# Performance work log

Hardware: AMD Instinct MI355X
Metric: run time of the kernel (lower is better)

The kernel has to match this reference:

```python
import jax, jax.numpy as jnp
import numpy as np
import math

HID = 1024; HEADS = 8; DH = 128; CS = 200; MAXPOS = 512; K = 15; EXP = 2; MULT = 4
SCALE = DH ** -0.5
CEXP = HID * EXP  # 2048 depthwise channels


def _ln(x, g, b, eps=1e-5):
    m = jnp.mean(x, axis=-1, keepdims=True)
    v = jnp.var(x, axis=-1, keepdims=True)
    return (x - m) * jax.lax.rsqrt(v + eps) * g + b


def _ff(x, ng, nb, w1, b1, w2, b2):
    h = jax.nn.silu(_ln(x, ng, nb) @ w1 + b1)
    return h @ w2 + b2


def _attn(x, dists, ng, nb, wq, wkv, pos_emb, wo, bo):
    B, N, _ = x.shape
    x = _ln(x, ng, nb)
    nblk = math.ceil(N / CS)
    rem = N % CS
    if rem:
        x = jnp.pad(x, ((0, 0), (0, CS - rem), (0, 0)))

    def heads(t):  # [B, M*C, H*Dh] -> [B, M, H, C, Dh]
        return t.reshape(B, nblk, CS, HEADS, DH).transpose(0, 1, 3, 2, 4)

    q = heads(x @ wq)
    k, v = jnp.split(x @ wkv, 2, axis=-1)
    k, v = heads(k), heads(v)
    rel = pos_emb[dists]  # [C, C, Dh] Shaw relative position embeddings
    pos_attn = jnp.einsum('bmhcd,crd->bmhcr', q, rel) * SCALE
    if rem:
        mask = jnp.ones((CS, CS), bool).at[:rem, :rem].set(False)
        big_neg = -jnp.finfo(pos_attn.dtype).max
        pos_attn = pos_attn.at[:, -1].set(jnp.where(mask, big_neg, pos_attn[:, -1]))
    scores = jnp.einsum('bmhcd,bmhrd->bmhcr', q, k) * SCALE + pos_attn
    p = jax.nn.softmax(scores, axis=-1)
    o = jnp.einsum('bmhcr,bmhrd->bmhcd', p, v)
    o = o.transpose(0, 1, 3, 2, 4).reshape(B, nblk * CS, HEADS * DH)[:, :N]
    return o @ wo + bo


def _conv(x, ng, nb, pw1_w, pw1_b, dw_w, bn_g, bn_b, bn_m, bn_v, pw2_w, pw2_b):
    h = _ln(x, ng, nb) @ pw1_w + pw1_b            # [B, N, 2*CEXP] pointwise conv1
    a, gate = jnp.split(h, 2, axis=-1)
    h = (a * jax.nn.sigmoid(gate)).transpose(0, 2, 1)  # GLU -> [B, CEXP, N]
    pad = (K - 1) // 2
    h = jax.lax.conv_general_dilated(h, dw_w[:, None, :], (1,), [(pad, pad)],
                                     feature_group_count=CEXP,
                                     dimension_numbers=('NCH', 'OIH', 'NCH'))
    # BatchNorm1d in eval mode (running stats)
    h = (h - bn_m[:, None]) * jax.lax.rsqrt(bn_v[:, None] + 1e-5) * bn_g[:, None] + bn_b[:, None]
    h = jax.nn.silu(h).transpose(0, 2, 1)
    return h @ pw2_w + pw2_b


def setup_inputs() -> dict:
    ks = iter(jax.random.split(jax.random.key(0), 16))
    def nrm(shape, s=0.05):
        return jax.random.normal(next(ks), shape, dtype=jnp.float32) * s
    return {
        'x': jax.random.normal(next(ks), (8, 2000, HID), dtype=jnp.float32),
        'attention_dists': jax.random.randint(next(ks), (CS, CS), 0, 2 * MAXPOS + 1),
        'ff1_ng': jnp.ones((HID,)), 'ff1_nb': jnp.zeros((HID,)),
        'ff1_w1': nrm((HID, HID * MULT)), 'ff1_b1': jnp.zeros((HID * MULT,)),
        'ff1_w2': nrm((HID * MULT, HID)), 'ff1_b2': jnp.zeros((HID,)),
        'attn_ng': jnp.ones((HID,)), 'attn_nb': jnp.zeros((HID,)),
        'wq': nrm((HID, HEADS * DH)), 'wkv': nrm((HID, 2 * HEADS * DH)),
        'pos_emb': nrm((2 * MAXPOS + 1, DH)),
        'wo': nrm((HEADS * DH, HID)), 'bo': jnp.zeros((HID,)),
        'conv_ng': jnp.ones((HID,)), 'conv_nb': jnp.zeros((HID,)),
        'pw1_w': nrm((HID, 2 * CEXP)), 'pw1_b': jnp.zeros((2 * CEXP,)),
        'dw_w': nrm((CEXP, K)),
        'bn_g': jnp.ones((CEXP,)), 'bn_b': jnp.zeros((CEXP,)),
        'bn_m': jnp.zeros((CEXP,)), 'bn_v': jnp.ones((CEXP,)),
        'pw2_w': nrm((CEXP, HID)), 'pw2_b': jnp.zeros((HID,)),
        'ff2_ng': jnp.ones((HID,)), 'ff2_nb': jnp.zeros((HID,)),
        'ff2_w1': nrm((HID, HID * MULT)), 'ff2_b1': jnp.zeros((HID * MULT,)),
        'ff2_w2': nrm((HID * MULT, HID)), 'ff2_b2': jnp.zeros((HID,)),
        'post_g': jnp.ones((HID,)), 'post_b': jnp.zeros((HID,)),
    }


def reference(x, attention_dists, ff1_ng, ff1_nb, ff1_w1, ff1_b1, ff1_w2, ff1_b2,
              attn_ng, attn_nb, wq, wkv, pos_emb, wo, bo,
              conv_ng, conv_nb, pw1_w, pw1_b, dw_w, bn_g, bn_b, bn_m, bn_v, pw2_w, pw2_b,
              ff2_ng, ff2_nb, ff2_w1, ff2_b1, ff2_w2, ff2_b2, post_g, post_b):
    x = x + 0.5 * _ff(x, ff1_ng, ff1_nb, ff1_w1, ff1_b1, ff1_w2, ff1_b2)
    x = x + _attn(x, attention_dists, attn_ng, attn_nb, wq, wkv, pos_emb, wo, bo)
    x = x + _conv(x, conv_ng, conv_nb, pw1_w, pw1_b, dw_w, bn_g, bn_b, bn_m, bn_v, pw2_w, pw2_b)
    x = x + 0.5 * _ff(x, ff2_ng, ff2_nb, ff2_w1, ff2_b1, ff2_w2, ff2_b2)
    return _ln(x, post_g, post_b)
```

## Files before the change

### kernel.cpp

```cpp
#include <hip/hip_runtime.h>
#include <hip/hip_bf16.h>
#include <stdint.h>

using bf16 = __hip_bfloat16;
typedef __bf16 bf16x8v __attribute__((ext_vector_type(8)));
typedef float f32x4 __attribute__((ext_vector_type(4)));

#define MFMA16(a,b,c) __builtin_amdgcn_mfma_f32_16x16x32_bf16((a),(b),(c),0,0,0)

__device__ __forceinline__ float tof(bf16 h){ return __bfloat162float(h); }
__device__ __forceinline__ bf16 tob(float f){ return __float2bfloat16(f); }

__device__ __forceinline__ void gll16(const void* g, void* l) {
    __builtin_amdgcn_global_load_lds((const __attribute__((address_space(1))) void*)g,
                                     (__attribute__((address_space(3))) void*)l, 16, 0, 0);
}

__global__ __launch_bounds__(256)
void pad_zero(bf16* __restrict__ q, bf16* __restrict__ k, bf16* __restrict__ v)
{
    int blk = blockIdx.x, t = threadIdx.x;
    uint2 z = make_uint2(0u, 0u);
    size_t qk = (size_t)blk * 208 * 128;
    int r = 200 + (t >> 5), c = (t & 31) * 4;
    *(uint2*)(q + qk + r*128 + c) = z;
    *(uint2*)(k + qk + r*128 + c) = z;
    size_t vb = (size_t)blk * 128 * 224;
    int d = t >> 1, c0 = 200 + (t & 1) * 12;
    *(uint2*)(v + vb + d*224 + c0)     = z;
    *(uint2*)(v + vb + d*224 + c0 + 4) = z;
    *(uint2*)(v + vb + d*224 + c0 + 8) = z;
}

__global__ __launch_bounds__(256)
void cast_pe(const float* __restrict__ in, bf16* __restrict__ out, int n8)
{
    int i = blockIdx.x * 256 + threadIdx.x;
    if (i >= n8) return;
    f32x4 a = ((const f32x4*)in)[2*i], b = ((const f32x4*)in)[2*i + 1];
    union { uint4 u; bf16 h[8]; } o;
#pragma unroll
    for (int j = 0; j < 4; ++j) { o.h[j] = tob(a[j]); o.h[4+j] = tob(b[j]); }
    ((uint4*)out)[i] = o.u;
}

__global__ __launch_bounds__(256)
void transpose_cast(const float* __restrict__ in, bf16* __restrict__ out, int R, int C)
{
    __shared__ float t[32][33];
    int bx = blockIdx.x * 32, by = blockIdx.y * 32;
    int tx = threadIdx.x & 31, ty = threadIdx.x >> 5;
#pragma unroll
    for (int i = 0; i < 4; ++i)
        t[ty + i*8][tx] = in[(size_t)(by + ty + i*8) * C + bx + tx];
    __syncthreads();
#pragma unroll
    for (int i = 0; i < 4; ++i)
        out[(size_t)(bx + ty + i*8) * R + by + tx] = tob(t[tx][ty + i*8]);
}

template<bool OUT32>
__global__ __launch_bounds__(256)
void ln_k(const float* __restrict__ x, const float* __restrict__ g,
          const float* __restrict__ b, void* __restrict__ out)
{
    int row = blockIdx.x, tid = threadIdx.x;
    const float4 v = ((const float4*)(x + (size_t)row*1024))[tid];
    float s = v.x + v.y + v.z + v.w;
    float q = v.x*v.x + v.y*v.y + v.z*v.z + v.w*v.w;
#pragma unroll
    for (int m = 1; m < 64; m <<= 1) { s += __shfl_xor(s, m); q += __shfl_xor(q, m); }
    __shared__ float red[8];
    if ((tid & 63) == 0) { red[tid>>6] = s; red[4 + (tid>>6)] = q; }
    __syncthreads();
    float ts = red[0]+red[1]+red[2]+red[3];
    float tq = red[4]+red[5]+red[6]+red[7];
    float mean = ts * (1.f/1024.f);
    float var  = tq * (1.f/1024.f) - mean*mean;
    float rs = rsqrtf(var + 1e-5f);
    const float4 gv = ((const float4*)g)[tid];
    const float4 bv = ((const float4*)b)[tid];
    float o0 = (v.x-mean)*rs*gv.x + bv.x;
    float o1 = (v.y-mean)*rs*gv.y + bv.y;
    float o2 = (v.z-mean)*rs*gv.z + bv.z;
    float o3 = (v.w-mean)*rs*gv.w + bv.w;
    if (OUT32) {
        ((float4*)out)[(size_t)row*256 + tid] = make_float4(o0,o1,o2,o3);
    } else {
        bf16 tmp[4] = { tob(o0), tob(o1), tob(o2), tob(o3) };
        ((uint2*)out)[(size_t)row*256 + tid] = *(const uint2*)tmp;
    }
}

template<int EP>
__global__ __launch_bounds__(256, 2)
void gemm_bt(const bf16* __restrict__ A, const bf16* __restrict__ BT,
             int M, int N, int K, int lda,
             const float* __restrict__ bias, const float* resid, float alpha,
             void* o0, void* o1, void* o2)
{
    (void)M;
    __shared__ bf16 sA[2][4096];
    __shared__ bf16 sB[2][4096];
    const int tid = threadIdx.x;
    const int lane = tid & 63, wid = tid >> 6;
    const int wm = wid >> 1, wn = wid & 1;
    const int bn0 = blockIdx.x * 128, bm0 = blockIdx.y * 128;
    const int fr = lane & 15, fq = lane >> 4;
    const int nk = K >> 5;

    f32x4 acc[4][4];
    const f32x4 vzero = {0.f, 0.f, 0.f, 0.f};
#pragma unroll
    for (int i = 0; i < 4; ++i)
#pragma unroll
        for (int j = 0; j < 4; ++j) acc[i][j] = vzero;

    const bf16* Abase = A + (size_t)bm0 * lda;
    const bf16* Bbase = BT + (size_t)bn0 * K;

    auto stage = [&](int kb, int buf) {
#pragma unroll
        for (int rd = 0; rd < 2; ++rd) {
            int s = rd*256 + tid;
            int r = s >> 2, ko = (s & 3) * 8;
            gll16(Abase + (size_t)r*lda + kb*32 + ko, &sA[buf][s*8]);
            gll16(Bbase + (size_t)r*K   + kb*32 + ko, &sB[buf][s*8]);
        }
    };

    stage(0, 0);
    for (int kb = 0; kb < nk; ++kb) {
        __syncthreads();
        if (kb + 1 < nk) stage(kb+1, (kb+1) & 1);
        const bf16* sa = sA[kb & 1];
        const bf16* sb = sB[kb & 1];
        bf16x8v af[4], bfv[4];
#pragma unroll
        for (int mi = 0; mi < 4; ++mi)
            af[mi] = *(const bf16x8v*)(sa + (wm*64 + mi*16 + fr)*32 + fq*8);
#pragma unroll
        for (int ni = 0; ni < 4; ++ni)
            bfv[ni] = *(const bf16x8v*)(sb + (wn*64 + ni*16 + fr)*32 + fq*8);
#pragma unroll
        for (int mi = 0; mi < 4; ++mi)
#pragma unroll
            for (int ni = 0; ni < 4; ++ni)
                acc[mi][ni] = MFMA16(af[mi], bfv[ni], acc[mi][ni]);
    }

#pragma unroll
    for (int mi = 0; mi < 4; ++mi)
#pragma unroll
    for (int ni = 0; ni < 4; ++ni)
#pragma unroll
    for (int r = 0; r < 4; ++r) {
        int row = bm0 + wm*64 + mi*16 + fq*4 + r;
        int col = bn0 + wn*64 + ni*16 + fr;
        float v = acc[mi][ni][r];
        if (EP == 0) {
            v += bias[col];
            v = v * (1.f / (1.f + __expf(-v)));
            ((bf16*)o0)[(size_t)row * N + col] = tob(v);
        } else if (EP == 1) {
            v += bias[col];
            ((bf16*)o0)[(size_t)row * N + col] = tob(v);
        } else if (EP == 2) {
            float o = resid[(size_t)row * N + col] + alpha * (v + bias[col]);
            ((float*)o0)[(size_t)row * N + col] = o;
        } else {
            int sec = col >> 10, hh = (col >> 7) & 7, d = col & 127;
            int blk = (row / 200) * 8 + hh, c = row % 200;
            if (sec == 0)      ((bf16*)o0)[((size_t)blk*208 + c)*128 + d] = tob(v * 0.08838834764831845f);
            else if (sec == 1) ((bf16*)o1)[((size_t)blk*208 + c)*128 + d] = tob(v);
            else               ((bf16*)o2)[((size_t)blk*128 + d)*224 + c] = tob(v);
        }
    }
}

__global__ __launch_bounds__(64)
void pos_kernel(const bf16* __restrict__ qb, const bf16* __restrict__ peb,
                const int* __restrict__ dists, bf16* __restrict__ pbuf)
{
    const int c = blockIdx.y, mt = blockIdx.x;
    const int lane = threadIdx.x;
    const int fr = lane & 15, fq = lane >> 4;
    bf16x8v qa[4][4];
#pragma unroll
    for (int sub = 0; sub < 4; ++sub)
#pragma unroll
        for (int kk = 0; kk < 4; ++kk)
            qa[sub][kk] = *(const bf16x8v*)(qb + ((size_t)(mt*64 + sub*16 + fr)*208 + c)*128 + kk*32 + fq*8);

    for (int rt = 0; rt < 13; ++rt) {
        int r = rt*16 + fr;
        int pidx = (r < 200) ? dists[c*200 + r] : 0;
        bf16x8v bv[4];
#pragma unroll
        for (int kk = 0; kk < 4; ++kk)
            bv[kk] = *(const bf16x8v*)(peb + (size_t)pidx*128 + kk*32 + fq*8);
#pragma unroll
        for (int sub = 0; sub < 4; ++sub) {
            f32x4 a = {0.f,0.f,0.f,0.f};
#pragma unroll
            for (int kk = 0; kk < 4; ++kk) a = MFMA16(qa[sub][kk], bv[kk], a);
            int bmh = mt*64 + sub*16 + fq*4;
#pragma unroll
            for (int g = 0; g < 4; ++g)
                pbuf[((size_t)c*640 + bmh + g)*208 + r] = tob(a[g]);
        }
    }
}

__global__ __launch_bounds__(64, 4)
void attn_core(const bf16* __restrict__ qb, const bf16* __restrict__ kb,
               const bf16* __restrict__ vt, const bf16* __restrict__ pb,
               bf16* __restrict__ ob)
{
    __shared__ bf16 P[16][232];
    const int blk = blockIdx.x, qc = blockIdx.y;
    const int lane = threadIdx.x;
    const int fr = lane & 15, fq = lane >> 4;
    const size_t qkbase = (size_t)blk * 208 * 128;
    const size_t vbase  = (size_t)blk * 128 * 224;
    const int c = qc*16 + fr;

    bf16x8v qa[4];
#pragma unroll
    for (int kk = 0; kk < 4; ++kk)
        qa[kk] = *(const bf16x8v*)(qb + qkbase + (size_t)(qc*16 + fr)*128 + kk*32 + fq*8);

    f32x4 s[13];
#pragma unroll
    for (int rt = 0; rt < 13; ++rt) {
        f32x4 a = {0.f,0.f,0.f,0.f};
#pragma unroll
        for (int kk = 0; kk < 4; ++kk) {
            bf16x8v kf = *(const bf16x8v*)(kb + qkbase + (size_t)(rt*16 + fr)*128 + kk*32 + fq*8);
            a = MFMA16(kf, qa[kk], a);
        }
        s[rt] = a;
    }
#pragma unroll
    for (int rt = 0; rt < 13; ++rt) {
        if (c < 200) {
            union { uint2 u; bf16 h[4]; } pv;
            pv.u = *(const uint2*)(pb + ((size_t)c*640 + blk)*208 + rt*16 + fq*4);
#pragma unroll
            for (int g = 0; g < 4; ++g) s[rt][g] += tof(pv.h[g]);
        }
        if (rt == 12 && fq >= 2) {
#pragma unroll
            for (int g = 0; g < 4; ++g)
                if (fq*4 + g >= 8) s[rt][g] = -1e30f;
        }
    }
    float mx = -3e38f;
#pragma unroll
    for (int rt = 0; rt < 13; ++rt)
#pragma unroll
        for (int g = 0; g < 4; ++g) mx = fmaxf(mx, s[rt][g]);
    mx = fmaxf(mx, __shfl_xor(mx, 16));
    mx = fmaxf(mx, __shfl_xor(mx, 32));
    float sm = 0.f;
#pragma unroll
    for (int rt = 0; rt < 13; ++rt)
#pragma unroll
        for (int g = 0; g < 4; ++g) { float pv = __expf(s[rt][g] - mx); s[rt][g] = pv; sm += pv; }
    sm += __shfl_xor(sm, 16);
    sm += __shfl_xor(sm, 32);
    float inv = 1.f / sm;
#pragma unroll
    for (int rt = 0; rt < 13; ++rt) {
        union { uint2 u; bf16 h[4]; } pw;
#pragma unroll
        for (int g = 0; g < 4; ++g) pw.h[g] = tob(s[rt][g] * inv);
        *(uint2*)&P[fr][rt*16 + fq*4] = pw.u;
    }
    *(uint2*)&P[fr][208 + fq*4] = make_uint2(0u, 0u);

    bf16x8v pa[7];
#pragma unroll
    for (int kt = 0; kt < 7; ++kt)
        pa[kt] = *(const bf16x8v*)(&P[fr][kt*32 + fq*8]);
#pragma unroll
    for (int nt = 0; nt < 8; ++nt) {
        f32x4 o = {0.f,0.f,0.f,0.f};
#pragma unroll
        for (int kt = 0; kt < 7; ++kt) {
            bf16x8v vf = *(const bf16x8v*)(vt + vbase + (size_t)(nt*16 + fr)*224 + kt*32 + fq*8);
            o = MFMA16(pa[kt], vf, o);
        }
        int d = nt*16 + fr;
#pragma unroll
        for (int g = 0; g < 4; ++g) {
            int cc = qc*16 + fq*4 + g;
            if (cc < 200)
                ob[((size_t)(blk >> 3)*200 + cc)*1024 + (blk & 7)*128 + d] = tob(o[g]);
        }
    }
}

__global__ __launch_bounds__(256)
void glu_k(bf16* __restrict__ h)
{
    size_t idx = (size_t)blockIdx.x*256 + threadIdx.x;
    size_t row = idx >> 8; int c0 = (int)(idx & 255) * 8;
    bf16* pa = h + row*4096 + c0;
    const bf16* pg = h + row*4096 + 2048 + c0;
    union { uint4 u; bf16 hh[8]; } a, g, o;
    a.u = *(const uint4*)pa; g.u = *(const uint4*)pg;
#pragma unroll
    for (int j = 0; j < 8; ++j) {
        float av = tof(a.hh[j]), gv = tof(g.hh[j]);
        o.hh[j] = tob(av * (1.f / (1.f + __expf(-gv))));
    }
    *(uint4*)pa = o.u;
}

__global__ __launch_bounds__(256)
void dwconv(const bf16* __restrict__ h, const float* __restrict__ dw,
            const float* __restrict__ bng, const float* __restrict__ bnb,
            const float* __restrict__ bnm, const float* __restrict__ bnv,
            bf16* __restrict__ out)
{
    int ch = blockIdx.x*256 + threadIdx.x;
    int b  = blockIdx.z;
    int n0 = blockIdx.y * 125;
    float wgt[15];
#pragma unroll
    for (int i = 0; i < 15; ++i) wgt[i] = dw[ch*15 + i];
    float sc = bng[ch] * rsqrtf(bnv[ch] + 1e-5f);
    float sh = bnb[ch] - bnm[ch]*sc;
    const size_t rowbase = (size_t)b*2000;
    float win[15];
#pragma unroll
    for (int i = 0; i < 15; ++i) {
        int nn = n0 - 7 + i;
        win[i] = (nn >= 0 && nn < 2000) ? tof(h[(rowbase + nn)*4096 + ch]) : 0.f;
    }
    for (int j = 0; j < 125; ++j) {
        int n = n0 + j;
        float a = 0.f;
#pragma unroll
        for (int i = 0; i < 15; ++i) a += win[i]*wgt[i];
        float y = a*sc + sh;
        y = y * (1.f / (1.f + __expf(-y)));
        out[(rowbase + n)*4096 + ch] = tob(y);
#pragma unroll
        for (int i = 0; i < 14; ++i) win[i] = win[i+1];
        int nn = n + 8;
        win[14] = (nn < 2000) ? tof(h[(rowbase + nn)*4096 + ch]) : 0.f;
    }
}

extern "C" void kernel_launch(void* const* d_in, const int* in_sizes, int n_in,
                              void* d_out, int out_size, void* d_ws, size_t ws_size,
                              hipStream_t stream)
{
    (void)in_sizes; (void)n_in; (void)out_size; (void)ws_size;
    const float* x      = (const float*)d_in[0];
    const int*   dists  = (const int*)d_in[1];
    const float* ff1_ng = (const float*)d_in[2];
    const float* ff1_nb = (const float*)d_in[3];
    const float* ff1_w1 = (const float*)d_in[4];
    const float* ff1_b1 = (const float*)d_in[5];
    const float* ff1_w2 = (const float*)d_in[6];
    const float* ff1_b2 = (const float*)d_in[7];
    const float* attn_ng= (const float*)d_in[8];
    const float* attn_nb= (const float*)d_in[9];
    const float* wq     = (const float*)d_in[10];
    const float* wkv    = (const float*)d_in[11];
    const float* pos_emb= (const float*)d_in[12];
    const float* wo     = (const float*)d_in[13];
    const float* bo     = (const float*)d_in[14];
    const float* conv_ng= (const float*)d_in[15];
    const float* conv_nb= (const float*)d_in[16];
    const float* pw1_w  = (const float*)d_in[17];
    const float* pw1_b  = (const float*)d_in[18];
    const float* dw_w   = (const float*)d_in[19];
    const float* bn_g   = (const float*)d_in[20];
    const float* bn_b   = (const float*)d_in[21];
    const float* bn_m   = (const float*)d_in[22];
    const float* bn_v   = (const float*)d_in[23];
    const float* pw2_w  = (const float*)d_in[24];
    const float* pw2_b  = (const float*)d_in[25];
    const float* ff2_ng = (const float*)d_in[26];
    const float* ff2_nb = (const float*)d_in[27];
    const float* ff2_w1 = (const float*)d_in[28];
    const float* ff2_b1 = (const float*)d_in[29];
    const float* ff2_w2 = (const float*)d_in[30];
    const float* ff2_b2 = (const float*)d_in[31];
    const float* post_g = (const float*)d_in[32];
    const float* post_b = (const float*)d_in[33];

    float* xres = (float*)d_out;

    char* p = (char*)d_ws;
    bf16*  xn    = (bf16*)p;   p += 32768000;
    bf16* ff1w1T = (bf16*)p;   p += 8388608;
    bf16* ff1w2T = (bf16*)p;   p += 8388608;
    bf16* qkvT   = (bf16*)p;   p += 6291456;
    bf16* woT    = (bf16*)p;   p += 2097152;
    bf16* pw1T   = (bf16*)p;   p += 8388608;
    bf16* pw2T   = (bf16*)p;   p += 4194304;
    bf16* ff2w1T = (bf16*)p;   p += 8388608;
    bf16* ff2w2T = (bf16*)p;   p += 8388608;
    bf16* peb    = (bf16*)p;   p += 262400;
    char* trans  = p;
    bf16* qbuf = (bf16*)trans;
    bf16* kbuf = qbuf + (size_t)640*208*128;
    bf16* vT   = kbuf + (size_t)640*208*128;
    bf16* posb = vT   + (size_t)640*128*224;
    bf16* hbuf = (bf16*)trans;

    transpose_cast<<<dim3(128, 32), 256, 0, stream>>>(ff1_w1, ff1w1T, 1024, 4096);
    transpose_cast<<<dim3(32, 128), 256, 0, stream>>>(ff1_w2, ff1w2T, 4096, 1024);
    transpose_cast<<<dim3(32, 32),  256, 0, stream>>>(wq, qkvT, 1024, 1024);
    transpose_cast<<<dim3(64, 32),  256, 0, stream>>>(wkv, qkvT + (size_t)1024*1024, 1024, 2048);
    transpose_cast<<<dim3(32, 32),  256, 0, stream>>>(wo, woT, 1024, 1024);
    transpose_cast<<<dim3(128, 32), 256, 0, stream>>>(pw1_w, pw1T, 1024, 4096);
    transpose_cast<<<dim3(32, 64),  256, 0, stream>>>(pw2_w, pw2T, 2048, 1024);
    transpose_cast<<<dim3(128, 32), 256, 0, stream>>>(ff2_w1, ff2w1T, 1024, 4096);
    transpose_cast<<<dim3(32, 128), 256, 0, stream>>>(ff2_w2, ff2w2T, 4096, 1024);
    cast_pe<<<65, 256, 0, stream>>>(pos_emb, peb, 16400);

    ln_k<false><<<16000, 256, 0, stream>>>(x, ff1_ng, ff1_nb, xn);
    gemm_bt<0><<<dim3(32,125), 256, 0, stream>>>(xn, ff1w1T, 16000,4096,1024,1024,
                                                 ff1_b1, nullptr, 0.f, hbuf, nullptr, nullptr);
    gemm_bt<2><<<dim3(8,125), 256, 0, stream>>>(hbuf, ff1w2T, 16000,1024,4096,4096,
                                                ff1_b2, x, 0.5f, xres, nullptr, nullptr);

    ln_k<false><<<16000, 256, 0, stream>>>(xres, attn_ng, attn_nb, xn);
    pad_zero<<<640, 256, 0, stream>>>(qbuf, kbuf, vT);
    gemm_bt<3><<<dim3(24,125), 256, 0, stream>>>(xn, qkvT, 16000,3072,1024,1024,
                                                 nullptr, nullptr, 0.f, qbuf, kbuf, vT);
    pos_kernel<<<dim3(10,200), 64, 0, stream>>>(qbuf, peb, dists, posb);
    attn_core<<<dim3(640,13), 64, 0, stream>>>(qbuf, kbuf, vT, posb, xn);
    gemm_bt<2><<<dim3(8,125), 256, 0, stream>>>(xn, woT, 16000,1024,1024,1024,
                                                bo, xres, 1.f, xres, nullptr, nullptr);

    ln_k<false><<<16000, 256, 0, stream>>>(xres, conv_ng, conv_nb, xn);
    gemm_bt<1><<<dim3(32,125), 256, 0, stream>>>(xn, pw1T, 16000,4096,1024,1024,
                                                 pw1_b, nullptr, 0.f, hbuf, nullptr, nullptr);
    glu_k<<<16000, 256, 0, stream>>>(hbuf);
    dwconv<<<dim3(8,16,8), 256, 0, stream>>>(hbuf, dw_w, bn_g, bn_b, bn_m, bn_v, hbuf + 2048);
    gemm_bt<2><<<dim3(8,125), 256, 0, stream>>>(hbuf + 2048, pw2T, 16000,1024,2048,4096,
                                                pw2_b, xres, 1.f, xres, nullptr, nullptr);

    ln_k<false><<<16000, 256, 0, stream>>>(xres, ff2_ng, ff2_nb, xn);
    gemm_bt<0><<<dim3(32,125), 256, 0, stream>>>(xn, ff2w1T, 16000,4096,1024,1024,
                                                 ff2_b1, nullptr, 0.f, hbuf, nullptr, nullptr);
    gemm_bt<2><<<dim3(8,125), 256, 0, stream>>>(hbuf, ff2w2T, 16000,1024,4096,4096,
                                                ff2_b2, xres, 0.5f, xres, nullptr, nullptr);

    ln_k<true><<<16000, 256, 0, stream>>>(xres, post_g, post_b, d_out);
}
```

Measured before the change: 1.877 ms.

## Replace 128x128 GEMM with 256x256 tiled, swizzled, phase-pipelined 8-wave kernel

Replaces the 128x128-tile, 256-thread GEMM with a 256x256-tile, 512-thread kernel. It stages 64-deep K slices into XOR-swizzled LDS in quarter chunks interleaved with four MFMA phases per K step, and uses s_setprio and explicit barriers to overlap loads with compute. Workgroup IDs are remapped across the 8 XCDs, and M is padded up to 63 row tiles with bounds checks on the residual and QKV epilogues. The goal is more reuse per loaded byte and better latency hiding, at the cost of one block per CU, higher register pressure, and padded-row work. The plain-store bf16 epilogues have no row check, but the enlarged xn buffer appears intended to absorb padded-row reads.

```diff
diff --git a/kernel.cpp b/kernel.cpp
--- a/kernel.cpp
+++ b/kernel.cpp
@@ -92,70 +92,110 @@
     }
 }
 
+#define PHASE(kt_, mh_, ks_, sqkt_, sqq_) do {                                   \
+    const int buf_ = (kt_) & 1;                                                  \
+    const char* sa_ = (const char*)&sA[buf_][0];                                 \
+    const char* sb_ = (const char*)&sB[buf_][0];                                 \
+    bf16x8v af_[4], bf_[4];                                                      \
+    _Pragma("unroll")                                                            \
+    for (int mi = 0; mi < 4; ++mi) {                                             \
+        int X = (wm*128 + (mh_)*64 + mi*16 + fr)*128 + (ks_)*64 + fq*16;         \
+        X ^= ((X >> 9) & 1) << 5;                                                \
+        af_[mi] = *(const bf16x8v*)(sa_ + X);                                    \
+    }                                                                            \
+    _Pragma("unroll")                                                            \
+    for (int ni = 0; ni < 4; ++ni) {                                             \
+        int X = (wn*64 + ni*16 + fr)*128 + (ks_)*64 + fq*16;                     \
+        X ^= ((X >> 9) & 1) << 5;                                                \
+        bf_[ni] = *(const bf16x8v*)(sb_ + X);                                    \
+    }                                                                            \
+    stageQ((sqkt_), (sqq_));                                                     \
+    __builtin_amdgcn_sched_barrier(0);                                           \
+    __builtin_amdgcn_s_barrier();                                                \
+    asm volatile("s_waitcnt lgkmcnt(0)" ::: "memory");                           \
+    __builtin_amdgcn_sched_barrier(0);                                           \
+    __builtin_amdgcn_s_setprio(1);                                               \
+    _Pragma("unroll")                                                            \
+    for (int mi = 0; mi < 4; ++mi)                                               \
+    _Pragma("unroll")                                                            \
+    for (int ni = 0; ni < 4; ++ni)                                               \
+        acc[(mh_)*4+mi][ni] = MFMA16(af_[mi], bf_[ni], acc[(mh_)*4+mi][ni]);     \
+    __builtin_amdgcn_s_setprio(0);                                               \
+    __builtin_amdgcn_sched_barrier(0);                                           \
+    __builtin_amdgcn_s_barrier();                                                \
+} while (0)
+
 template<int EP>
-__global__ __launch_bounds__(256, 2)
-void gemm_bt(const bf16* __restrict__ A, const bf16* __restrict__ BT,
+__global__ __launch_bounds__(512, 1)
+void gemm256(const bf16* __restrict__ A, const bf16* __restrict__ BT,
              int M, int N, int K, int lda,
              const float* __restrict__ bias, const float* resid, float alpha,
              void* o0, void* o1, void* o2)
 {
-    (void)M;
-    __shared__ bf16 sA[2][4096];
-    __shared__ bf16 sB[2][4096];
+    __shared__ bf16 sA[2][16384];
+    __shared__ bf16 sB[2][16384];
     const int tid = threadIdx.x;
     const int lane = tid & 63, wid = tid >> 6;
-    const int wm = wid >> 1, wn = wid & 1;
-    const int bn0 = blockIdx.x * 128, bm0 = blockIdx.y * 128;
+    const int wm = wid >> 2, wn = wid & 3;
     const int fr = lane & 15, fq = lane >> 4;
-    const int nk = K >> 5;
-
-    f32x4 acc[4][4];
+    const int nk = K >> 6;
+
+    const int nwg = gridDim.x, bid = blockIdx.x;
+    const int xcd = bid & 7, idx = bid >> 3;
+    const int q8 = nwg >> 3, r8 = nwg & 7;
+    const int wg = (xcd < r8 ? xcd*(q8+1) : r8*(q8+1) + (xcd - r8)*q8) + idx;
+    const int Nt = N >> 8;
+    const int bm0 = (wg / Nt) << 8;
+    const int bn0 = (wg % Nt) << 8;
+
+    f32x4 acc[8][4];
     const f32x4 vzero = {0.f, 0.f, 0.f, 0.f};
 #pragma unroll
-    for (int i = 0; i < 4; ++i)
+    for (int i = 0; i < 8; ++i)
 #pragma unroll
         for (int j = 0; j < 4; ++j) acc[i][j] = vzero;
 
     const bf16* Abase = A + (size_t)bm0 * lda;
     const bf16* Bbase = BT + (size_t)bn0 * K;
 
-    auto stage = [&](int kb, int buf) {
-#pragma unroll
-        for (int rd = 0; rd < 2; ++rd) {
-            int s = rd*256 + tid;
-            int r = s >> 2, ko = (s & 3) * 8;
-            gll16(Abase + (size_t)r*lda + kb*32 + ko, &sA[buf][s*8]);
-            gll16(Bbase + (size_t)r*K   + kb*32 + ko, &sB[buf][s*8]);
+    auto stageQ = [&](int kt, int q) {
+        if (kt >= nk) return;
+        const int buf = kt & 1;
+        char* dst = (char*)(q < 2 ? &sA[buf][0] : &sB[buf][0]);
+        const int half = q & 1;
+#pragma unroll
+        for (int l = 0; l < 2; ++l) {
+            int Y = half*16384 + (l*512 + tid)*16;
+            int lin = Y ^ (((Y >> 9) & 1) << 5);
+            int srow = lin >> 7;
+            int scol = (lin & 127) >> 1;
+            const bf16* g = (q < 2)
+                ? Abase + (size_t)srow * lda + kt*64 + scol
+                : Bbase + (size_t)srow * K   + kt*64 + scol;
+            gll16(g, dst + Y);
         }
     };
 
-    stage(0, 0);
-    for (int kb = 0; kb < nk; ++kb) {
-        __syncthreads();
-        if (kb + 1 < nk) stage(kb+1, (kb+1) & 1);
-        const bf16* sa = sA[kb & 1];
-        const bf16* sb = sB[kb & 1];
-        bf16x8v af[4], bfv[4];
-#pragma unroll
-        for (int mi = 0; mi < 4; ++mi)
-            af[mi] = *(const bf16x8v*)(sa + (wm*64 + mi*16 + fr)*32 + fq*8);
-#pragma unroll
-        for (int ni = 0; ni < 4; ++ni)
-            bfv[ni] = *(const bf16x8v*)(sb + (wn*64 + ni*16 + fr)*32 + fq*8);
-#pragma unroll
-        for (int mi = 0; mi < 4; ++mi)
-#pragma unroll
-            for (int ni = 0; ni < 4; ++ni)
-                acc[mi][ni] = MFMA16(af[mi], bfv[ni], acc[mi][ni]);
-    }
-
-#pragma unroll
-    for (int mi = 0; mi < 4; ++mi)
+    stageQ(0,0); stageQ(0,1); stageQ(0,2); stageQ(0,3);
+    stageQ(1,0);
+
+    for (int kt = 0; kt < nk; ++kt) {
+        asm volatile("s_waitcnt vmcnt(2)" ::: "memory");
+        __builtin_amdgcn_sched_barrier(0);
+        __builtin_amdgcn_s_barrier();
+        PHASE(kt, 0, 0, kt+1, 1);
+        PHASE(kt, 0, 1, kt+1, 2);
+        PHASE(kt, 1, 0, kt+1, 3);
+        PHASE(kt, 1, 1, kt+2, 0);
+    }
+
+#pragma unroll
+    for (int mi = 0; mi < 8; ++mi)
 #pragma unroll
     for (int ni = 0; ni < 4; ++ni)
 #pragma unroll
     for (int r = 0; r < 4; ++r) {
-        int row = bm0 + wm*64 + mi*16 + fq*4 + r;
+        int row = bm0 + wm*128 + mi*16 + fq*4 + r;
         int col = bn0 + wn*64 + ni*16 + fr;
         float v = acc[mi][ni][r];
         if (EP == 0) {
@@ -166,14 +206,18 @@
             v += bias[col];
             ((bf16*)o0)[(size_t)row * N + col] = tob(v);
         } else if (EP == 2) {
-            float o = resid[(size_t)row * N + col] + alpha * (v + bias[col]);
-            ((float*)o0)[(size_t)row * N + col] = o;
+            if (row < M) {
+                float o = resid[(size_t)row * N + col] + alpha * (v + bias[col]);
+                ((float*)o0)[(size_t)row * N + col] = o;
+            }
         } else {
-            int sec = col >> 10, hh = (col >> 7) & 7, d = col & 127;
-            int blk = (row / 200) * 8 + hh, c = row % 200;
-            if (sec == 0)      ((bf16*)o0)[((size_t)blk*208 + c)*128 + d] = tob(v * 0.08838834764831845f);
-            else if (sec == 1) ((bf16*)o1)[((size_t)blk*208 + c)*128 + d] = tob(v);
-            else               ((bf16*)o2)[((size_t)blk*128 + d)*224 + c] = tob(v);
+            if (row < M) {
+                int sec = col >> 10, hh = (col >> 7) & 7, d = col & 127;
+                int blk = (row / 200) * 8 + hh, c = row % 200;
+                if (sec == 0)      ((bf16*)o0)[((size_t)blk*208 + c)*128 + d] = tob(v * 0.08838834764831845f);
+                else if (sec == 1) ((bf16*)o1)[((size_t)blk*208 + c)*128 + d] = tob(v);
+                else               ((bf16*)o2)[((size_t)blk*128 + d)*224 + c] = tob(v);
+            }
         }
     }
 }
@@ -397,7 +441,7 @@
     float* xres = (float*)d_out;
 
     char* p = (char*)d_ws;
-    bf16*  xn    = (bf16*)p;   p += 32768000;
+    bf16*  xn    = (bf16*)p;   p += 33030144;
     bf16* ff1w1T = (bf16*)p;   p += 8388608;
     bf16* ff1w2T = (bf16*)p;   p += 8388608;
     bf16* qkvT   = (bf16*)p;   p += 6291456;
@@ -426,33 +470,33 @@
     cast_pe<<<65, 256, 0, stream>>>(pos_emb, peb, 16400);
 
     ln_k<false><<<16000, 256, 0, stream>>>(x, ff1_ng, ff1_nb, xn);
-    gemm_bt<0><<<dim3(32,125), 256, 0, stream>>>(xn, ff1w1T, 16000,4096,1024,1024,
-                                                 ff1_b1, nullptr, 0.f, hbuf, nullptr, nullptr);
-    gemm_bt<2><<<dim3(8,125), 256, 0, stream>>>(hbuf, ff1w2T, 16000,1024,4096,4096,
-                                                ff1_b2, x, 0.5f, xres, nullptr, nullptr);
+    gemm256<0><<<63*16, 512, 0, stream>>>(xn, ff1w1T, 16000,4096,1024,1024,
+                                          ff1_b1, nullptr, 0.f, hbuf, nullptr, nullptr);
+    gemm256<2><<<63*4, 512, 0, stream>>>(hbuf, ff1w2T, 16000,1024,4096,4096,
+                                         ff1_b2, x, 0.5f, xres, nullptr, nullptr);
 
     ln_k<false><<<16000, 256, 0, stream>>>(xres, attn_ng, attn_nb, xn);
     pad_zero<<<640, 256, 0, stream>>>(qbuf, kbuf, vT);
-    gemm_bt<3><<<dim3(24,125), 256, 0, stream>>>(xn, qkvT, 16000,3072,1024,1024,
-                                                 nullptr, nullptr, 0.f, qbuf, kbuf, vT);
+    gemm256<3><<<63*12, 512, 0, stream>>>(xn, qkvT, 16000,3072,1024,1024,
+                                          nullptr, nullptr, 0.f, qbuf, kbuf, vT);
     pos_kernel<<<dim3(10,200), 64, 0, stream>>>(qbuf, peb, dists, posb);
     attn_core<<<dim3(640,13), 64, 0, stream>>>(qbuf, kbuf, vT, posb, xn);
-    gemm_bt<2><<<dim3(8,125), 256, 0, stream>>>(xn, woT, 16000,1024,1024,1024,
-                                                bo, xres, 1.f, xres, nullptr, nullptr);
+    gemm256<2><<<63*4, 512, 0, stream>>>(xn, woT, 16000,1024,1024,1024,
+                                         bo, xres, 1.f, xres, nullptr, nullptr);
 
     ln_k<false><<<16000, 256, 0, stream>>>(xres, conv_ng, conv_nb, xn);
-    gemm_bt<1><<<dim3(32,125), 256, 0, stream>>>(xn, pw1T, 16000,4096,1024,1024,
-                                                 pw1_b, nullptr, 0.f, hbuf, nullptr, nullptr);
+    gemm256<1><<<63*16, 512, 0, stream>>>(xn, pw1T, 16000,4096,1024,1024,
+                                          pw1_b, nullptr, 0.f, hbuf, nullptr, nullptr);
     glu_k<<<16000, 256, 0, stream>>>(hbuf);
     dwconv<<<dim3(8,16,8), 256, 0, stream>>>(hbuf, dw_w, bn_g, bn_b, bn_m, bn_v, hbuf + 2048);
-    gemm_bt<2><<<dim3(8,125), 256, 0, stream>>>(hbuf + 2048, pw2T, 16000,1024,2048,4096,
-                                                pw2_b, xres, 1.f, xres, nullptr, nullptr);
+    gemm256<2><<<63*4, 512, 0, stream>>>(hbuf + 2048, pw2T, 16000,1024,2048,4096,
+                                         pw2_b, xres, 1.f, xres, nullptr, nullptr);
 
     ln_k<false><<<16000, 256, 0, stream>>>(xres, ff2_ng, ff2_nb, xn);
-    gemm_bt<0><<<dim3(32,125), 256, 0, stream>>>(xn, ff2w1T, 16000,4096,1024,1024,
-                                                 ff2_b1, nullptr, 0.f, hbuf, nullptr, nullptr);
-    gemm_bt<2><<<dim3(8,125), 256, 0, stream>>>(hbuf, ff2w2T, 16000,1024,4096,4096,
-                                                ff2_b2, xres, 0.5f, xres, nullptr, nullptr);
+    gemm256<0><<<63*16, 512, 0, stream>>>(xn, ff2w1T, 16000,4096,1024,1024,
+                                          ff2_b1, nullptr, 0.f, hbuf, nullptr, nullptr);
+    gemm256<2><<<63*4, 512, 0, stream>>>(hbuf, ff2w2T, 16000,1024,4096,4096,
+                                         ff2_b2, xres, 0.5f, xres, nullptr, nullptr);
 
     ln_k<true><<<16000, 256, 0, stream>>>(xres, post_g, post_b, d_out);
 }
```

Result: slower. 1.923 ms (+2.5%).
